# Kernel optimization log

Measured on AMD Instinct MI355X. Metric: run time of the kernel, lower is better.

## Reference

```python
import jax, jax.numpy as jnp
import numpy as np

N = 50000   # nodes
E = 200000  # edges per relation
R = 4       # relations
IN = 128
HID = 32
H = 4
OUT = 32


def setup_inputs() -> dict:
    key = jax.random.key(0)
    ks = jax.random.split(key, 32)
    w = lambda k, shape: jax.random.normal(k, shape, jnp.float32) * 0.05
    inp = {
        "x": jax.random.normal(ks[0], (N, IN), jnp.float32),
        "edge_src": jax.random.randint(ks[1], (R, E), 0, N, dtype=jnp.int32),
        "edge_dst": jax.random.randint(ks[2], (R, E), 0, N, dtype=jnp.int32),
    }
    # (d_in, heads*d_out, d_out) per layer: flatten, flatten, mean-over-heads
    dims = [(IN, H * HID, HID), (H * HID, H * HID, HID), (H * HID, H * OUT, OUT)]
    i = 3
    for l, (din, dout, d) in enumerate(dims):
        inp[f"Wsrc{l}"] = w(ks[i], (R, din, dout)); i += 1
        inp[f"bsrc{l}"] = w(ks[i], (R, dout)); i += 1
        inp[f"Wdst{l}"] = w(ks[i], (R, din, dout)); i += 1
        inp[f"bdst{l}"] = w(ks[i], (R, dout)); i += 1
        inp[f"attn{l}"] = w(ks[i], (R, H, d)); i += 1
    return inp


def rel_gatv2(h, src, dst, Ws, bs, Wd, bd, att):
    """DGL GATv2Conv for one relation: gather, leaky-relu score, edge softmax, scatter-sum."""
    n = h.shape[0]
    heads, d = att.shape
    fs = (h @ Ws + bs).reshape(n, heads, d)   # [N,H,D]
    fd = (h @ Wd + bd).reshape(n, heads, d)
    e = jax.nn.leaky_relu(fs[src] + fd[dst], 0.2)        # [E,H,D]
    score = jnp.einsum('ehd,hd->eh', e, att)             # [E,H]
    # numerically stable edge softmax segmented by destination node
    m = jax.lax.stop_gradient(jax.ops.segment_max(score, dst, num_segments=n))
    m = jnp.where(jnp.isfinite(m), m, 0.0)               # zero-in-degree guard
    ex = jnp.exp(score - m[dst])
    den = jax.ops.segment_sum(ex, dst, num_segments=n)
    a = ex / jnp.maximum(den[dst], 1e-16)                # [E,H]
    return jax.ops.segment_sum(a[:, :, None] * fs[src], dst, num_segments=n)  # [N,H,D]


def gat_layer(h, edge_src, edge_dst, Ws, bs, Wd, bd, att, mean_heads):
    out = None
    for r in range(Ws.shape[0]):  # small fixed relation count; HeteroGraphConv sums
        o = rel_gatv2(h, edge_src[r], edge_dst[r], Ws[r], bs[r], Wd[r], bd[r], att[r])
        out = o if out is None else out + o
    if mean_heads:                # last_layer_flag: mean over heads
        return out.mean(axis=1)
    return out.reshape(h.shape[0], -1)  # flatten heads


def reference(x, edge_src, edge_dst,
              Wsrc0, bsrc0, Wdst0, bdst0, attn0,
              Wsrc1, bsrc1, Wdst1, bdst1, attn1,
              Wsrc2, bsrc2, Wdst2, bdst2, attn2):
    h = gat_layer(x, edge_src, edge_dst, Wsrc0, bsrc0, Wdst0, bdst0, attn0, False)
    h = gat_layer(h, edge_src, edge_dst, Wsrc1, bsrc1, Wdst1, bdst1, attn1, False)
    h = gat_layer(h, edge_src, edge_dst, Wsrc2, bsrc2, Wdst2, bdst2, attn2, True)
    return h  # [N, OUT]
```

## Files before the change

kernel.cpp:

```cpp
#include <hip/hip_runtime.h>
#include <math.h>

#define FF 128
#define G0F 1024
#define GG 2048
#define BSH 8
#define CAPB 256

typedef _Float16 half2v __attribute__((ext_vector_type(2)));
typedef _Float16 f16x8  __attribute__((ext_vector_type(8)));
typedef __fp16   fp16x2 __attribute__((ext_vector_type(2)));
typedef __attribute__((ext_vector_type(4))) float f4v;

__device__ __forceinline__ half2v u2h(unsigned u) {
    union { unsigned u; half2v h; } c; c.u = u; return c.h;
}
__device__ __forceinline__ unsigned h2u(half2v h) {
    union { unsigned u; half2v h; } c; c.h = h; return c.u;
}
__device__ __forceinline__ unsigned short f2h(float f) {
    _Float16 h = (_Float16)f;
    unsigned short u; __builtin_memcpy(&u, &h, 2); return u;
}
__device__ __forceinline__ half2v pk2h(float e) {
    union { fp16x2 p; half2v h; } c;
    c.p = __builtin_amdgcn_cvt_pkrtz(e, e);
    return c.h;
}
__device__ __forceinline__ float dot2(half2v a, half2v b, float c) {
#if __has_builtin(__builtin_amdgcn_fdot2)
    union { half2v h; fp16x2 p; } ca, cb;
    ca.h = a; cb.h = b;
    return __builtin_amdgcn_fdot2(ca.p, cb.p, c, false);
#else
    return c + (float)a.x * (float)b.x + (float)a.y * (float)b.y;
#endif
}
__device__ __forceinline__ half2v shfladd_h(half2v v, int mask) {
    return v + u2h(__shfl_xor(h2u(v), mask));
}
__device__ __forceinline__ int swz16(int row, int chunk) {
    return row * 256 + (((chunk ^ row) & 15) << 4);
}


__global__ __launch_bounds__(256) void pack0(
    const float* __restrict__ W0s_, const float* __restrict__ W0d_,
    unsigned short* __restrict__ Wp,
    const float* __restrict__ a0, const float* __restrict__ a1,
    const float* __restrict__ a2, unsigned* __restrict__ attH)
{
    int b = blockIdx.x;
    const int tid = threadIdx.x;
    if (b < 512) {
        const int t = b * 256 + tid;
        const int r   = t >> 15;
        const int mat = (t >> 14) & 1;
        const int idx = t & 16383;
        const int k = idx >> 7, nn = idx & 127;
        const float* W = mat ? W0d_ : W0s_;
        const float v = W[((size_t)r * FF + k) * FF + nn];
        const int nb = nn >> 4, lo = nn & 15;
        const int ks = k >> 5, quad = (k >> 3) & 3, j = k & 7;
        const int lane = quad * 16 + lo;
        const size_t o = ((((((size_t)r * 2 + mat) * 8 + nb) * 4 + ks) * 64 + lane) * 8) + j;
        Wp[o] = f2h(v);
        return;
    }
    b -= 512;
    const int t = b * 256 + tid;
    if (t >= 768) return;
    const int l = t >> 8, rest = t & 255;
    const float* a = (l == 0) ? a0 : (l == 1) ? a1 : a2;
    const float2 v = ((const float2*)a)[rest];
    half2v h = {(_Float16)v.x, (_Float16)v.y};
    attH[t] = h2u(h);
}

__global__ __launch_bounds__(256, 4) void fused3(
    const int* __restrict__ esrc_all, const int* __restrict__ edst_all,
    int* __restrict__ bcur, unsigned* __restrict__ bbuf,
    int totalE, int ne, int n, int NB, int CB2,
    const float* __restrict__ x,
    const unsigned short* __restrict__ Wp,
    const float* __restrict__ bs0, const float* __restrict__ bd0,
    unsigned short* __restrict__ fs_all, unsigned short* __restrict__ fd_all,
    int nrb,
    const float* __restrict__ W1s_, const float* __restrict__ W1d_,
    const float* __restrict__ W2s_, const float* __restrict__ W2d_,
    unsigned short* __restrict__ Wp_full)
{
    __shared__ char lsA[4096];
    __shared__ char lsC[8192];

    int b = blockIdx.x;
    const int tid = threadIdx.x;

    if (b < CB2) {
        const int part = b & 7;
        const int t0 = b * 1024 + tid;
        #pragma unroll
        for (int k = 0; k < 4; ++k) {
            const int i = t0 + k * 256;
            if (i < totalE) {
                const int r = i / ne;
                const int rd = r * n + edst_all[i];
                const int src = esrc_all[i];
                const int bkt = rd >> BSH;
                const int reg = part * NB + bkt;
                const int pos = atomicAdd(&bcur[reg << 4], 1);
                if (pos < CAPB)
                    bbuf[((size_t)reg << 8) + pos] =
                        ((unsigned)(rd & 255) << 16) | (unsigned)src;
            }
        }
        return;
    }
    b -= CB2;

    if (b < G0F) {
        const int wave = tid >> 6, lane = tid & 63;
        const int r = b & 3;
        const int half = wave & 1;
        const int mat  = wave >> 1;
        const int lo = lane & 15, quad = lane >> 4;

        const unsigned short* Wr = Wp + (size_t)r * 2 * FF * FF;
        const float* bp = mat ? bd0 : bs0;
        unsigned short* fs = fs_all + (size_t)r * n * FF;
        unsigned short* fd = fd_all + (size_t)r * n * FF;

        f16x8 B[4][4];
        #pragma unroll
        for (int nbi = 0; nbi < 4; ++nbi)
            #pragma unroll
            for (int ks = 0; ks < 4; ++ks) {
                const int nb = half * 4 + nbi;
                B[nbi][ks] = *(const f16x8*)
                    &Wr[(((((size_t)mat * 8 + nb) * 4 + ks) * 64 + lane) * 8)];
            }

        float bias[4];
        #pragma unroll
        for (int nbi = 0; nbi < 4; ++nbi)
            bias[nbi] = bp[r * FF + (half * 4 + nbi) * 16 + lo];

        const int srow = tid >> 4, schunk = tid & 15;
        const int stride = G0F >> 2;
        for (int rb = b >> 2; rb < nrb; rb += stride) {
            const int row0 = rb * 16;
            {
                const float* xs = &x[(size_t)row0 * FF + tid * 8];
                const float4 p0 = *(const float4*)&xs[0];
                const float4 p1 = *(const float4*)&xs[4];
                f16x8 v;
                v[0] = (_Float16)p0.x; v[1] = (_Float16)p0.y;
                v[2] = (_Float16)p0.z; v[3] = (_Float16)p0.w;
                v[4] = (_Float16)p1.x; v[5] = (_Float16)p1.y;
                v[6] = (_Float16)p1.z; v[7] = (_Float16)p1.w;
                *(f16x8*)&lsA[swz16(srow, schunk)] = v;
            }
            __syncthreads();

            f16x8 A[4];
            #pragma unroll
            for (int ks = 0; ks < 4; ++ks)
                A[ks] = *(const f16x8*)&lsA[swz16(lo, ks * 4 + quad)];

            f4v c[4];
            #pragma unroll
            for (int nbi = 0; nbi < 4; ++nbi)
                c[nbi] = (f4v){bias[nbi], bias[nbi], bias[nbi], bias[nbi]};

            #pragma unroll
            for (int ks = 0; ks < 4; ++ks)
                #pragma unroll
                for (int nbi = 0; nbi < 4; ++nbi)
                    c[nbi] = __builtin_amdgcn_mfma_f32_16x16x32_f16(
                        A[ks], B[nbi][ks], c[nbi], 0, 0, 0);

            #pragma unroll
            for (int nbi = 0; nbi < 4; ++nbi)
                #pragma unroll
                for (int i = 0; i < 4; ++i) {
                    const int row = quad * 4 + i;
                    const int cb  = ((half * 4 + nbi) * 16 + lo) * 2;
                    *(unsigned short*)&lsC[mat * 4096 + swz16(row, cb >> 4) + (cb & 15)]
                        = f2h(c[nbi][i]);
                }
            __syncthreads();

            #pragma unroll
            for (int p = 0; p < 2; ++p) {
                const int unit = p * 256 + tid;
                const int m    = unit >> 8;
                const int row  = (unit >> 4) & 15;
                const int ch   = unit & 15;
                const uint4 d = *(const uint4*)&lsC[m * 4096 + swz16(row, ch)];
                unsigned short* out = m ? fd : fs;
                *(uint4*)&out[(size_t)(row0 + row) * FF + ch * 8] = d;
            }
            __syncthreads();
        }
        return;
    }
    b -= G0F;

    const int t = b * 256 + tid;
    if (t >= 2 * 4 * 2 * FF * FF) return;
    const int l    = 1 + (t >> 17);
    const int rest = t & 131071;
    const int r    = rest >> 15;
    const int mat  = (rest >> 14) & 1;
    const int idx  = rest & 16383;
    const int k = idx >> 7, nn = idx & 127;
    const float* W = (l == 1) ? (mat ? W1d_ : W1s_)
                              : (mat ? W2d_ : W2s_);
    const float v = W[((size_t)r * FF + k) * FF + nn];
    const int nb = nn >> 4, lo = nn & 15;
    const int ks = k >> 5, quad = (k >> 3) & 3, j = k & 7;
    const int lane = quad * 16 + lo;
    const size_t o = (((((((size_t)l * 4 + r) * 2 + mat) * 8 + nb) * 4 + ks) * 64 + lane) * 8) + j;
    Wp_full[o] = f2h(v);
}

__global__ __launch_bounds__(256) void p3build(
    const int* __restrict__ bcur, const unsigned* __restrict__ bbuf,
    int* __restrict__ rec, int* __restrict__ ovf, int NB, int L)
{
    __shared__ int lrec[256 * 17];
    const int b = blockIdx.x;
    const int tid = threadIdx.x;

    #pragma unroll
    for (int k = 0; k < 17; ++k) lrec[k * 256 + tid] = 0;
    __syncthreads();

    const int rd0 = b << BSH;
    for (int part = 0; part < 8; ++part) {
        const int reg = part * NB + b;
        int c = bcur[reg << 4];
        c = c < CAPB ? c : CAPB;
        const unsigned* seg = &bbuf[(size_t)reg << 8];
        for (int e = tid; e < c; e += 256) {
            const unsigned v = seg[e];
            const int rdL = v >> 16;
            const int src = (int)(v & 0xFFFFu);
            const int idx = atomicAdd(&lrec[rdL * 17], 1);
            if (idx < 15)      lrec[rdL * 17 + 1 + idx] = src;
            else if (idx < 32) ovf[(size_t)(idx - 15) * L + rd0 + rdL] = src;
        }
    }
    __syncthreads();

    if (rd0 + tid < L) {
        int* out = &rec[(size_t)(rd0 + tid) * 16];
        #pragma unroll
        for (int w = 0; w < 4; ++w) {
            int4 d;
            d.x = lrec[tid * 17 + w * 4 + 0];
            d.y = lrec[tid * 17 + w * 4 + 1];
            d.z = lrec[tid * 17 + w * 4 + 2];
            d.w = lrec[tid * 17 + w * 4 + 3];
            *(int4*)&out[w * 4] = d;
        }
    }
}

__global__ __launch_bounds__(256, 4) void mfma_gemm(
    const unsigned short* __restrict__ hb,
    const unsigned short* __restrict__ Wp,
    const float* __restrict__ bs_all,
    const float* __restrict__ bd_all,
    unsigned short* __restrict__ fs_all,
    unsigned short* __restrict__ fd_all,
    int nrb, int n)
{
    __shared__ char lsA[4096];
    __shared__ char lsC[8192];

    const int tid = threadIdx.x;
    const int wave = tid >> 6, lane = tid & 63;
    const int r = blockIdx.x & 3;
    const int half = wave & 1;
    const int mat  = wave >> 1;
    const int lo = lane & 15, quad = lane >> 4;

    const unsigned short* Wr = Wp + (size_t)r * 2 * FF * FF;
    const float* bp = mat ? bd_all : bs_all;
    unsigned short* fs = fs_all + (size_t)r * n * FF;
    unsigned short* fd = fd_all + (size_t)r * n * FF;

    f16x8 B[4][4];
    #pragma unroll
    for (int nbi = 0; nbi < 4; ++nbi)
        #pragma unroll
        for (int ks = 0; ks < 4; ++ks) {
            const int nb = half * 4 + nbi;
            B[nbi][ks] = *(const f16x8*)
                &Wr[(((((size_t)mat * 8 + nb) * 4 + ks) * 64 + lane) * 8)];
        }

    float bias[4];
    #pragma unroll
    for (int nbi = 0; nbi < 4; ++nbi)
        bias[nbi] = bp[r * FF + (half * 4 + nbi) * 16 + lo];

    const int srow = tid >> 4, schunk = tid & 15;
    const int stride = gridDim.x >> 2;
    for (int rb = blockIdx.x >> 2; rb < nrb; rb += stride) {
        const int row0 = rb * 16;
        {
            const uint4 g = *(const uint4*)&hb[(size_t)row0 * FF + tid * 8];
            *(uint4*)&lsA[swz16(srow, schunk)] = g;
        }
        __syncthreads();

        f16x8 A[4];
        #pragma unroll
        for (int ks = 0; ks < 4; ++ks)
            A[ks] = *(const f16x8*)&lsA[swz16(lo, ks * 4 + quad)];

        f4v c[4];
        #pragma unroll
        for (int nbi = 0; nbi < 4; ++nbi)
            c[nbi] = (f4v){bias[nbi], bias[nbi], bias[nbi], bias[nbi]};

        #pragma unroll
        for (int ks = 0; ks < 4; ++ks)
            #pragma unroll
            for (int nbi = 0; nbi < 4; ++nbi)
                c[nbi] = __builtin_amdgcn_mfma_f32_16x16x32_f16(
                    A[ks], B[nbi][ks], c[nbi], 0, 0, 0);

        #pragma unroll
        for (int nbi = 0; nbi < 4; ++nbi)
            #pragma unroll
            for (int i = 0; i < 4; ++i) {
                const int row = quad * 4 + i;
                const int cb  = ((half * 4 + nbi) * 16 + lo) * 2;
                *(unsigned short*)&lsC[mat * 4096 + swz16(row, cb >> 4) + (cb & 15)]
                    = f2h(c[nbi][i]);
            }
        __syncthreads();

        #pragma unroll
        for (int p = 0; p < 2; ++p) {
            const int unit = p * 256 + tid;
            const int m    = unit >> 8;
            const int row  = (unit >> 4) & 15;
            const int ch   = unit & 15;
            const uint4 d = *(const uint4*)&lsC[m * 4096 + swz16(row, ch)];
            unsigned short* out = m ? fd : fs;
            *(uint4*)&out[(size_t)(row0 + row) * FF + ch * 8] = d;
        }
        __syncthreads();
    }
}

__device__ __forceinline__ void edge4(
    uint4 g, bool ok, const half2v* fdv, const half2v* atv,
    float& den, half2v* acc)
{
    const half2v C02 = {(_Float16)0.2f, (_Float16)0.2f};
    half2v f[4] = {u2h(g.x), u2h(g.y), u2h(g.z), u2h(g.w)};
    float v = 0.f;
    #pragma unroll
    for (int i = 0; i < 4; ++i) {
        const half2v z = f[i] + fdv[i];
        const half2v l = __builtin_elementwise_max(z, z * C02);
        v = dot2(l, atv[i], v);
    }
    v += __shfl_xor(v, 2);
    v += __shfl_xor(v, 1);
    const float e = ok ? __expf(v) : 0.f;
    den += e;
    const half2v eh = pk2h(e);
    #pragma unroll
    for (int i = 0; i < 4; ++i) acc[i] += eh * f[i];
}

__global__ __launch_bounds__(256) void aggregate(
    const int* __restrict__ rec,
    const int* __restrict__ ovf,
    const unsigned* __restrict__ fs_all,
    const unsigned* __restrict__ fd_all,
    const unsigned* __restrict__ att_h,
    unsigned* __restrict__ out_h,
    float* __restrict__ out_f32,
    int n)
{
    const int node = blockIdx.x * 4 + (threadIdx.x >> 6);
    if (node >= n) return;
    const int lane = threadIdx.x & 63;
    const int quarter = lane >> 4;
    const int q = lane & 15;
    const int fo = 4 * q;
    const int L = n << 2;

    int m[4], i0[4], i1[4];
    #pragma unroll
    for (int r = 0; r < 4; ++r) {
        const int rd = r * n + node;
        const int* rp = &rec[(size_t)rd * 16];
        m[r]  = rp[0];
        i0[r] = rp[1 + quarter];
        i1[r] = rp[5 + quarter];
    }

    half2v val[4];
    #pragma unroll
    for (int i = 0; i < 4; ++i) val[i] = (half2v){(_Float16)0.f, (_Float16)0.f};

    #pragma unroll
    for (int rp2 = 0; rp2 < 2; ++rp2) {
        const int ra = 2 * rp2, rb = 2 * rp2 + 1;
        const int rdA = ra * n + node;
        const int rdB = rb * n + node;
        const int mA = m[ra], mB = m[rb];
        const unsigned* fsuA = fs_all + (size_t)ra * n * 64;
        const unsigned* fsuB = fs_all + (size_t)rb * n * 64;

        const uint4 ufdA = *(const uint4*)&fd_all[(size_t)rdA * 64 + fo];
        const uint4 ufdB = *(const uint4*)&fd_all[(size_t)rdB * 64 + fo];
        const uint4 uatA = *(const uint4*)&att_h[ra * 64 + fo];
        const uint4 uatB = *(const uint4*)&att_h[rb * 64 + fo];

        const bool okA0 = quarter < mA, okA1 = 4 + quarter < mA;
        const bool okB0 = quarter < mB, okB1 = 4 + quarter < mB;
        int iA0 = okA0 ? i0[ra] : 0;
        int iB0 = okB0 ? i0[rb] : 0;
        int iA1 = okA1 ? i1[ra] : 0;
        int iB1 = okB1 ? i1[rb] : 0;
        const uint4 gA0 = *(const uint4*)&fsuA[(size_t)iA0 * 64 + fo];
        const uint4 gB0 = *(const uint4*)&fsuB[(size_t)iB0 * 64 + fo];
        const uint4 gA1 = *(const uint4*)&fsuA[(size_t)iA1 * 64 + fo];
        const uint4 gB1 = *(const uint4*)&fsuB[(size_t)iB1 * 64 + fo];

        half2v fdvA[4] = {u2h(ufdA.x), u2h(ufdA.y), u2h(ufdA.z), u2h(ufdA.w)};
        half2v atvA[4] = {u2h(uatA.x), u2h(uatA.y), u2h(uatA.z), u2h(uatA.w)};
        half2v fdvB[4] = {u2h(ufdB.x), u2h(ufdB.y), u2h(ufdB.z), u2h(ufdB.w)};
        half2v atvB[4] = {u2h(uatB.x), u2h(uatB.y), u2h(uatB.z), u2h(uatB.w)};

        float denA = 0.f, denB = 0.f;
        half2v accA[4], accB[4];
        #pragma unroll
        for (int i = 0; i < 4; ++i) {
            accA[i] = (half2v){(_Float16)0.f, (_Float16)0.f};
            accB[i] = (half2v){(_Float16)0.f, (_Float16)0.f};
        }

        edge4(gA0, okA0, fdvA, atvA, denA, accA);
        edge4(gB0, okB0, fdvB, atvB, denB, accB);
        if (mA > 4) edge4(gA1, okA1, fdvA, atvA, denA, accA);
        if (mB > 4) edge4(gB1, okB1, fdvB, atvB, denB, accB);

        if (mA > 8) {
            for (int p = 8; p < mA; p += 4) {
                const int ei = p + quarter;
                const bool ok = ei < mA;
                const int eic = ei < 31 ? ei : 31;
                int s = (eic < 15) ? rec[(size_t)rdA * 16 + 1 + eic]
                                   : ovf[(size_t)(eic - 15) * L + rdA];
                s = ok ? s : 0;
                const uint4 g = *(const uint4*)&fsuA[(size_t)s * 64 + fo];
                edge4(g, ok, fdvA, atvA, denA, accA);
            }
        }
        if (mB > 8) {
            for (int p = 8; p < mB; p += 4) {
                const int ei = p + quarter;
                const bool ok = ei < mB;
                const int eic = ei < 31 ? ei : 31;
                int s = (eic < 15) ? rec[(size_t)rdB * 16 + 1 + eic]
                                   : ovf[(size_t)(eic - 15) * L + rdB];
                s = ok ? s : 0;
                const uint4 g = *(const uint4*)&fsuB[(size_t)s * 64 + fo];
                edge4(g, ok, fdvB, atvB, denB, accB);
            }
        }

        if (mA) {
            denA += __shfl_xor(denA, 16);
            denA += __shfl_xor(denA, 32);
            const half2v ih = pk2h(__builtin_amdgcn_rcpf(denA));
            #pragma unroll
            for (int i = 0; i < 4; ++i) val[i] += accA[i] * ih;
        }
        if (mB) {
            denB += __shfl_xor(denB, 16);
            denB += __shfl_xor(denB, 32);
            const half2v ih = pk2h(__builtin_amdgcn_rcpf(denB));
            #pragma unroll
            for (int i = 0; i < 4; ++i) val[i] += accB[i] * ih;
        }
    }

    #pragma unroll
    for (int i = 0; i < 4; ++i) {
        val[i] = shfladd_h(val[i], 16);
        val[i] = shfladd_h(val[i], 32);
    }

    if (out_f32) {
        #pragma unroll
        for (int i = 0; i < 4; ++i) {
            val[i] = shfladd_h(val[i], 4);
            val[i] = shfladd_h(val[i], 8);
        }
        if (lane < 4) {
            float* o = &out_f32[(size_t)node * 32 + 8 * lane];
            *(float4*)&o[0] = make_float4(0.25f * (float)val[0].x, 0.25f * (float)val[0].y,
                                          0.25f * (float)val[1].x, 0.25f * (float)val[1].y);
            *(float4*)&o[4] = make_float4(0.25f * (float)val[2].x, 0.25f * (float)val[2].y,
                                          0.25f * (float)val[3].x, 0.25f * (float)val[3].y);
        }
    } else {
        if (lane < 16) {
            uint4 o;
            o.x = h2u(val[0]); o.y = h2u(val[1]);
            o.z = h2u(val[2]); o.w = h2u(val[3]);
            *(uint4*)&out_h[(size_t)node * 64 + fo] = o;
        }
    }
}

extern "C" void kernel_launch(void* const* d_in, const int* in_sizes, int n_in,
                              void* d_out, int out_size, void* d_ws, size_t ws_size,
                              hipStream_t stream)
{
    const int n  = in_sizes[0] / FF;
    const int R  = 4;
    const int ne = in_sizes[1] / R;
    const int totalE = R * ne;
    const int L  = R * n;
    const int nrb = (n + 15) / 16;
    const int NB = (L + 255) >> BSH;

    const float* x    = (const float*)d_in[0];
    const int*   esrc = (const int*)d_in[1];
    const int*   edst = (const int*)d_in[2];

    char* p = (char*)d_ws;
    auto carve = [&p](size_t bytes) { char* q = p; p += (bytes + 255) & ~(size_t)255; return q; };
    unsigned*       hbA    = (unsigned*)      carve((size_t)n * 64 * 4);
    unsigned*       hbB    = (unsigned*)      carve((size_t)n * 64 * 4);
    unsigned short* fs_all = (unsigned short*)carve((size_t)R * n * FF * 2);
    unsigned short* fd_all = (unsigned short*)carve((size_t)R * n * FF * 2);
    unsigned short* Wp     = (unsigned short*)carve((size_t)3 * R * 2 * FF * FF * 2);
    unsigned*       attH   = (unsigned*)      carve((size_t)3 * R * 64 * 4);
    int*            rec    = (int*)           carve((size_t)L * 16 * 4);
    int*            ovf    = (int*)           carve((size_t)17 * L * 4);
    int*            bcur   = (int*)           carve((size_t)8 * NB * 16 * 4);
    unsigned*       bbuf   = (unsigned*)      carve((size_t)8 * NB * CAPB * 4);

    (void)hipMemsetAsync(bcur, 0, (size_t)8 * NB * 16 * sizeof(int), stream);

    pack0<<<515, 256, 0, stream>>>(
        (const float*)d_in[3], (const float*)d_in[5], Wp,
        (const float*)d_in[7], (const float*)d_in[12], (const float*)d_in[17],
        attH);

    const int CB2 = (totalE + 1023) / 1024;
    fused3<<<CB2 + G0F + 1024, 256, 0, stream>>>(
        esrc, edst, bcur, bbuf, totalE, ne, n, NB, CB2,
        x, Wp,
        (const float*)d_in[4], (const float*)d_in[6],
        fs_all, fd_all, nrb,
        (const float*)d_in[8],  (const float*)d_in[10],
        (const float*)d_in[13], (const float*)d_in[15],
        Wp);

    p3build<<<NB, 256, 0, stream>>>(bcur, bbuf, rec, ovf, NB, L);

    unsigned* bufs[3] = {hbA, hbB, nullptr};
    for (int l = 0; l < 3; ++l) {
        if (l > 0) {
            const float* bsrc = (const float*)d_in[3 + 5 * l + 1];
            const float* bdst = (const float*)d_in[3 + 5 * l + 3];
            mfma_gemm<<<GG, 256, 0, stream>>>(
                (const unsigned short*)bufs[l - 1],
                Wp + (size_t)l * R * 2 * FF * FF,
                bsrc, bdst, fs_all, fd_all, nrb, n);
        }
        const int last = (l == 2);
        aggregate<<<(n + 3) / 4, 256, 0, stream>>>(
            rec, ovf,
            (const unsigned*)fs_all, (const unsigned*)fd_all,
            attH + (size_t)l * R * 64,
            last ? nullptr : bufs[l],
            last ? (float*)d_out : nullptr, n);
    }
}
```

Measured before the change: 377.9 us.

## Split aggregation relations across two waves per node, reduce via LDS

The aggregate kernel previously used one wave per node to process all four relations in two sequential passes. Now each node gets two waves, each handling one pair of relations, and the partial results are combined through shared memory after a block barrier. This doubles wave-level parallelism and shortens each wave's dependent gather chain to hide memory latency. In exchange it adds a __syncthreads, an LDS round-trip and a second wave's share of fd/att loads, and the grid doubles in size.

```diff
diff --git a/kernel.cpp b/kernel.cpp
--- a/kernel.cpp
+++ b/kernel.cpp
@@ -390,110 +390,105 @@
     float* __restrict__ out_f32,
     int n)
 {
-    const int node = blockIdx.x * 4 + (threadIdx.x >> 6);
-    if (node >= n) return;
-    const int lane = threadIdx.x & 63;
+    __shared__ uint4 lval[2][16];
+    const int tid = threadIdx.x;
+    const int wave = tid >> 6;
+    const int nib  = wave >> 1;
+    const int pair = wave & 1;
+    int node = blockIdx.x * 2 + nib;
+    const bool oknode = node < n;
+    if (!oknode) node = 0;
+    const int lane = tid & 63;
     const int quarter = lane >> 4;
     const int q = lane & 15;
     const int fo = 4 * q;
     const int L = n << 2;
 
-    int m[4], i0[4], i1[4];
+    const int ra = 2 * pair, rb = 2 * pair + 1;
+    const int rdA = ra * n + node;
+    const int rdB = rb * n + node;
+    const int* rpA = &rec[(size_t)rdA * 16];
+    const int* rpB = &rec[(size_t)rdB * 16];
+    const int mA = rpA[0], mB = rpB[0];
+    const int i0A = rpA[1 + quarter], i1A = rpA[5 + quarter];
+    const int i0B = rpB[1 + quarter], i1B = rpB[5 + quarter];
+
+    const unsigned* fsuA = fs_all + (size_t)ra * n * 64;
+    const unsigned* fsuB = fs_all + (size_t)rb * n * 64;
+
+    const uint4 ufdA = *(const uint4*)&fd_all[(size_t)rdA * 64 + fo];
+    const uint4 ufdB = *(const uint4*)&fd_all[(size_t)rdB * 64 + fo];
+    const uint4 uatA = *(const uint4*)&att_h[ra * 64 + fo];
+    const uint4 uatB = *(const uint4*)&att_h[rb * 64 + fo];
+
+    const bool okA0 = quarter < mA, okA1 = 4 + quarter < mA;
+    const bool okB0 = quarter < mB, okB1 = 4 + quarter < mB;
+    const int iA0 = okA0 ? i0A : 0;
+    const int iB0 = okB0 ? i0B : 0;
+    const int iA1 = okA1 ? i1A : 0;
+    const int iB1 = okB1 ? i1B : 0;
+    const uint4 gA0 = *(const uint4*)&fsuA[(size_t)iA0 * 64 + fo];
+    const uint4 gB0 = *(const uint4*)&fsuB[(size_t)iB0 * 64 + fo];
+    const uint4 gA1 = *(const uint4*)&fsuA[(size_t)iA1 * 64 + fo];
+    const uint4 gB1 = *(const uint4*)&fsuB[(size_t)iB1 * 64 + fo];
+
+    half2v fdvA[4] = {u2h(ufdA.x), u2h(ufdA.y), u2h(ufdA.z), u2h(ufdA.w)};
+    half2v atvA[4] = {u2h(uatA.x), u2h(uatA.y), u2h(uatA.z), u2h(uatA.w)};
+    half2v fdvB[4] = {u2h(ufdB.x), u2h(ufdB.y), u2h(ufdB.z), u2h(ufdB.w)};
+    half2v atvB[4] = {u2h(uatB.x), u2h(uatB.y), u2h(uatB.z), u2h(uatB.w)};
+
+    float denA = 0.f, denB = 0.f;
+    half2v accA[4], accB[4], val[4];
     #pragma unroll
-    for (int r = 0; r < 4; ++r) {
-        const int rd = r * n + node;
-        const int* rp = &rec[(size_t)rd * 16];
-        m[r]  = rp[0];
-        i0[r] = rp[1 + quarter];
-        i1[r] = rp[5 + quarter];
-    }
-
-    half2v val[4];
-    #pragma unroll
-    for (int i = 0; i < 4; ++i) val[i] = (half2v){(_Float16)0.f, (_Float16)0.f};
-
-    #pragma unroll
-    for (int rp2 = 0; rp2 < 2; ++rp2) {
-        const int ra = 2 * rp2, rb = 2 * rp2 + 1;
-        const int rdA = ra * n + node;
-        const int rdB = rb * n + node;
-        const int mA = m[ra], mB = m[rb];
-        const unsigned* fsuA = fs_all + (size_t)ra * n * 64;
-        const unsigned* fsuB = fs_all + (size_t)rb * n * 64;
-
-        const uint4 ufdA = *(const uint4*)&fd_all[(size_t)rdA * 64 + fo];
-        const uint4 ufdB = *(const uint4*)&fd_all[(size_t)rdB * 64 + fo];
-        const uint4 uatA = *(const uint4*)&att_h[ra * 64 + fo];
-        const uint4 uatB = *(const uint4*)&att_h[rb * 64 + fo];
-
-        const bool okA0 = quarter < mA, okA1 = 4 + quarter < mA;
-        const bool okB0 = quarter < mB, okB1 = 4 + quarter < mB;
-        int iA0 = okA0 ? i0[ra] : 0;
-        int iB0 = okB0 ? i0[rb] : 0;
-        int iA1 = okA1 ? i1[ra] : 0;
-        int iB1 = okB1 ? i1[rb] : 0;
-        const uint4 gA0 = *(const uint4*)&fsuA[(size_t)iA0 * 64 + fo];
-        const uint4 gB0 = *(const uint4*)&fsuB[(size_t)iB0 * 64 + fo];
-        const uint4 gA1 = *(const uint4*)&fsuA[(size_t)iA1 * 64 + fo];
-        const uint4 gB1 = *(const uint4*)&fsuB[(size_t)iB1 * 64 + fo];
-
-        half2v fdvA[4] = {u2h(ufdA.x), u2h(ufdA.y), u2h(ufdA.z), u2h(ufdA.w)};
-        half2v atvA[4] = {u2h(uatA.x), u2h(uatA.y), u2h(uatA.z), u2h(uatA.w)};
-        half2v fdvB[4] = {u2h(ufdB.x), u2h(ufdB.y), u2h(ufdB.z), u2h(ufdB.w)};
-        half2v atvB[4] = {u2h(uatB.x), u2h(uatB.y), u2h(uatB.z), u2h(uatB.w)};
-
-        float denA = 0.f, denB = 0.f;
-        half2v accA[4], accB[4];
-        #pragma unroll
-        for (int i = 0; i < 4; ++i) {
-            accA[i] = (half2v){(_Float16)0.f, (_Float16)0.f};
-            accB[i] = (half2v){(_Float16)0.f, (_Float16)0.f};
-        }
-
-        edge4(gA0, okA0, fdvA, atvA, denA, accA);
-        edge4(gB0, okB0, fdvB, atvB, denB, accB);
-        if (mA > 4) edge4(gA1, okA1, fdvA, atvA, denA, accA);
-        if (mB > 4) edge4(gB1, okB1, fdvB, atvB, denB, accB);
-
-        if (mA > 8) {
-            for (int p = 8; p < mA; p += 4) {
-                const int ei = p + quarter;
-                const bool ok = ei < mA;
-                const int eic = ei < 31 ? ei : 31;
-                int s = (eic < 15) ? rec[(size_t)rdA * 16 + 1 + eic]
-                                   : ovf[(size_t)(eic - 15) * L + rdA];
-                s = ok ? s : 0;
-                const uint4 g = *(const uint4*)&fsuA[(size_t)s * 64 + fo];
-                edge4(g, ok, fdvA, atvA, denA, accA);
-            }
-        }
-        if (mB > 8) {
-            for (int p = 8; p < mB; p += 4) {
-                const int ei = p + quarter;
-                const bool ok = ei < mB;
-                const int eic = ei < 31 ? ei : 31;
-                int s = (eic < 15) ? rec[(size_t)rdB * 16 + 1 + eic]
-                                   : ovf[(size_t)(eic - 15) * L + rdB];
-                s = ok ? s : 0;
-                const uint4 g = *(const uint4*)&fsuB[(size_t)s * 64 + fo];
-                edge4(g, ok, fdvB, atvB, denB, accB);
-            }
-        }
-
-        if (mA) {
-            denA += __shfl_xor(denA, 16);
-            denA += __shfl_xor(denA, 32);
-            const half2v ih = pk2h(__builtin_amdgcn_rcpf(denA));
-            #pragma unroll
-            for (int i = 0; i < 4; ++i) val[i] += accA[i] * ih;
-        }
-        if (mB) {
-            denB += __shfl_xor(denB, 16);
-            denB += __shfl_xor(denB, 32);
-            const half2v ih = pk2h(__builtin_amdgcn_rcpf(denB));
-            #pragma unroll
-            for (int i = 0; i < 4; ++i) val[i] += accB[i] * ih;
-        }
+    for (int i = 0; i < 4; ++i) {
+        accA[i] = (half2v){(_Float16)0.f, (_Float16)0.f};
+        accB[i] = (half2v){(_Float16)0.f, (_Float16)0.f};
+        val[i]  = (half2v){(_Float16)0.f, (_Float16)0.f};
+    }
+
+    edge4(gA0, okA0, fdvA, atvA, denA, accA);
+    edge4(gB0, okB0, fdvB, atvB, denB, accB);
+    if (mA > 4) edge4(gA1, okA1, fdvA, atvA, denA, accA);
+    if (mB > 4) edge4(gB1, okB1, fdvB, atvB, denB, accB);
+
+    if (mA > 8) {
+        for (int p = 8; p < mA; p += 4) {
+            const int ei = p + quarter;
+            const bool ok = ei < mA;
+            const int eic = ei < 31 ? ei : 31;
+            int s = (eic < 15) ? rec[(size_t)rdA * 16 + 1 + eic]
+                               : ovf[(size_t)(eic - 15) * L + rdA];
+            s = ok ? s : 0;
+            const uint4 g = *(const uint4*)&fsuA[(size_t)s * 64 + fo];
+            edge4(g, ok, fdvA, atvA, denA, accA);
+        }
+    }
+    if (mB > 8) {
+        for (int p = 8; p < mB; p += 4) {
+            const int ei = p + quarter;
+            const bool ok = ei < mB;
+            const int eic = ei < 31 ? ei : 31;
+            int s = (eic < 15) ? rec[(size_t)rdB * 16 + 1 + eic]
+                               : ovf[(size_t)(eic - 15) * L + rdB];
+            s = ok ? s : 0;
+            const uint4 g = *(const uint4*)&fsuB[(size_t)s * 64 + fo];
+            edge4(g, ok, fdvB, atvB, denB, accB);
+        }
+    }
+
+    if (mA) {
+        denA += __shfl_xor(denA, 16);
+        denA += __shfl_xor(denA, 32);
+        const half2v ih = pk2h(__builtin_amdgcn_rcpf(denA));
+        #pragma unroll
+        for (int i = 0; i < 4; ++i) val[i] += accA[i] * ih;
+    }
+    if (mB) {
+        denB += __shfl_xor(denB, 16);
+        denB += __shfl_xor(denB, 32);
+        const half2v ih = pk2h(__builtin_amdgcn_rcpf(denB));
+        #pragma unroll
+        for (int i = 0; i < 4; ++i) val[i] += accB[i] * ih;
     }
 
     #pragma unroll
@@ -502,13 +497,28 @@
         val[i] = shfladd_h(val[i], 32);
     }
 
+    if (pair == 1 && lane < 16) {
+        uint4 o;
+        o.x = h2u(val[0]); o.y = h2u(val[1]);
+        o.z = h2u(val[2]); o.w = h2u(val[3]);
+        lval[nib][q] = o;
+    }
+    __syncthreads();
+    if (pair != 0) return;
+
+    if (lane < 16) {
+        const uint4 o = lval[nib][q];
+        val[0] += u2h(o.x); val[1] += u2h(o.y);
+        val[2] += u2h(o.z); val[3] += u2h(o.w);
+    }
+
     if (out_f32) {
         #pragma unroll
         for (int i = 0; i < 4; ++i) {
             val[i] = shfladd_h(val[i], 4);
             val[i] = shfladd_h(val[i], 8);
         }
-        if (lane < 4) {
+        if (lane < 4 && oknode) {
             float* o = &out_f32[(size_t)node * 32 + 8 * lane];
             *(float4*)&o[0] = make_float4(0.25f * (float)val[0].x, 0.25f * (float)val[0].y,
                                           0.25f * (float)val[1].x, 0.25f * (float)val[1].y);
@@ -516,7 +526,7 @@
                                           0.25f * (float)val[3].x, 0.25f * (float)val[3].y);
         }
     } else {
-        if (lane < 16) {
+        if (lane < 16 && oknode) {
             uint4 o;
             o.x = h2u(val[0]); o.y = h2u(val[1]);
             o.z = h2u(val[2]); o.w = h2u(val[3]);
@@ -584,7 +594,7 @@
                 bsrc, bdst, fs_all, fd_all, nrb, n);
         }
         const int last = (l == 2);
-        aggregate<<<(n + 3) / 4, 256, 0, stream>>>(
+        aggregate<<<(n + 1) / 2, 256, 0, stream>>>(
             rec, ovf,
             (const unsigned*)fs_all, (const unsigned*)fd_all,
             attH + (size_t)l * R * 64,
```

New measurement: 385.3 us. No clear change (+2.0%).
